# Optimization experiments

Measured on AMD Instinct MI355X. Metric: run time of the kernel, lower is better.

The kernel has to match this reference:

```python
import jax, jax.numpy as jnp
import numpy as np

NG, N, NFG, NFR, NFP, B = 4, 64, 1024, 256, 256, 2048
SCALE = 1.0 / float(np.sqrt(NFR + NFP))
EPS = 1e-5  # torch LayerNorm default


def setup_inputs() -> dict:
    key = jax.random.key(0)
    k = jax.random.split(key, 4)
    x = jax.random.normal(k[0], (B, N, NFG), dtype=jnp.float32)
    # per-graph params stacked over NG for vectorized computation
    Wt = jax.random.normal(k[1], (NG, NFR, NFG), dtype=jnp.float32) * 0.02
    bt = jnp.zeros((NG, NFR), dtype=jnp.float32)
    Wp = jax.random.normal(k[2], (NG, NFR, NFG), dtype=jnp.float32) * 0.02
    bp = jnp.zeros((NG, NFR), dtype=jnp.float32)
    Wg = jax.random.normal(k[3], (NG, NFG, NFG), dtype=jnp.float32) * 0.02  # [out,in]
    gamma = jnp.ones((NG, NFG), dtype=jnp.float32)
    beta = jnp.zeros((NG, NFG), dtype=jnp.float32)
    return {"x": x, "Wt": Wt, "bt": bt, "Wp": Wp, "bp": bp,
            "Wg": Wg, "gamma": gamma, "beta": beta}


def reference(x, Wt, bt, Wp, bp, Wg, gamma, beta):
    # theta/phi projections, vectorized over NG graphs: [G,B,N,R]
    theta = jnp.einsum('bnf,grf->gbnr', x, Wt) + bt[:, None, None, :]
    phi = jnp.einsum('bnf,grf->gbnr', x, Wp) + bp[:, None, None, :]
    # original computes sim=theta@phi^T then .sum(2); identical math:
    # relation[b,n] = theta[b,n] . sum_m phi[b,m]  (avoids the NxN matrix)
    phi_sum = phi.sum(axis=2)                                  # [G,B,R]
    relation = jnp.einsum('gbnr,gbr->gbn', theta, phi_sum) * SCALE
    w = jax.nn.softmax(relation, axis=2)                       # softmax over boxes N
    # attention-weighted aggregation over boxes -> [G,B,NFG]
    agg = jnp.einsum('gbn,bnf->gbf', w, x)
    # GCN linear (no bias): [G,B,NFG]
    h = jnp.einsum('gbf,gof->gbo', agg, Wg)
    # LayerNorm over feature dim, per graph
    mu = h.mean(axis=-1, keepdims=True)
    var = ((h - mu) ** 2).mean(axis=-1, keepdims=True)
    h = (h - mu) * jax.lax.rsqrt(var + EPS) * gamma[:, None, :] + beta[:, None, :]
    h = jax.nn.relu(h)
    # mean over the NG graphs; restore keepdim axis -> [B,1,NFG]
    return h.mean(axis=0)[:, None, :]
```

## Files before the change

kernel.cpp:

```cpp
#include <hip/hip_runtime.h>
#include <hip/hip_bf16.h>

typedef __attribute__((ext_vector_type(4))) float f4;
typedef __attribute__((ext_vector_type(4))) float f32x4;
typedef __attribute__((ext_vector_type(8))) short short8;
typedef __attribute__((ext_vector_type(2))) unsigned int u32x2;
typedef __attribute__((ext_vector_type(4))) unsigned int u32x4;
typedef unsigned int u32;
typedef unsigned short u16;

#define SCALE_F 0.04419417382415922f

__device__ inline u16 f2bf(float f) {
  u32 u = __float_as_uint(f);
  u32 r = u + 0x7FFFu + ((u >> 16) & 1u);
  return (u16)(r >> 16);
}
__device__ inline float bflo(u32 u) { return __uint_as_float(u << 16); }
__device__ inline float bfhi(u32 u) { return __uint_as_float(u & 0xFFFF0000u); }

#define GLD16(gsrc, ldst)                                                     \
  __builtin_amdgcn_global_load_lds(                                           \
      (const __attribute__((address_space(1))) void*)(gsrc),                  \
      (__attribute__((address_space(3))) void*)(ldst), 16, 0, 0)

__global__ __launch_bounds__(256) void k0_cvt(const float* __restrict__ src,
                                              u16* __restrict__ dst) {
  int i = blockIdx.x * 256 + threadIdx.x;
  const f4* s = (const f4*)src;
  f4 a = s[(size_t)i * 2];
  f4 b = s[(size_t)i * 2 + 1];
  u32x4 p;
  p[0] = (u32)f2bf(a[0]) | ((u32)f2bf(a[1]) << 16);
  p[1] = (u32)f2bf(a[2]) | ((u32)f2bf(a[3]) << 16);
  p[2] = (u32)f2bf(b[0]) | ((u32)f2bf(b[1]) << 16);
  p[3] = (u32)f2bf(b[2]) | ((u32)f2bf(b[3]) << 16);
  *(u32x4*)(dst + (size_t)i * 8) = p;
}

__global__ __launch_bounds__(256) void k0_wt(const float* __restrict__ Wt,
                                             u16* __restrict__ Wtt) {
  const int g = blockIdx.z;
  const int f0 = blockIdx.x * 64, r0 = blockIdx.y * 64;
  __shared__ u16 tile[64][66];
  const int t = threadIdx.x;
  const float* src = Wt + ((size_t)g * 256 + r0) * 1024 + f0;
#pragma unroll
  for (int i = 0; i < 16; ++i) {
    int idx = t + i * 256;
    int rl = idx >> 6, fl = idx & 63;
    tile[fl][rl] = f2bf(src[rl * 1024 + fl]);
  }
  __syncthreads();
  u16* dst = Wtt + ((size_t)g * 1024 + f0) * 256 + r0;
#pragma unroll
  for (int i = 0; i < 4; ++i) {
    int idx = t + i * 256;
    int fl = idx >> 4, rq = idx & 15;
    u32x2 p;
    p[0] = (u32)tile[fl][rq * 4]     | ((u32)tile[fl][rq * 4 + 1] << 16);
    p[1] = (u32)tile[fl][rq * 4 + 2] | ((u32)tile[fl][rq * 4 + 3] << 16);
    *(u32x2*)(dst + fl * 256 + rq * 4) = p;
  }
}

__global__ __launch_bounds__(256) void k1_prep(const float* __restrict__ x,
                                               u16* __restrict__ xs16,
                                               char* __restrict__ xpre) {
  const int b = blockIdx.x, t = threadIdx.x;
  const float* xb = x + (size_t)b * 65536;
  char* xp = xpre + (size_t)b * 131072;
  const int slot = t >> 1, half = t & 1;
  f4 acc = {0.f, 0.f, 0.f, 0.f};
#pragma unroll 8
  for (int n = 0; n < 64; ++n) {
    f4 v = *(const f4*)(xb + n * 1024 + t * 4);
    acc += v;
    u32 p0 = (u32)f2bf(v[0]) | ((u32)f2bf(v[1]) << 16);
    u32 p1 = (u32)f2bf(v[2]) | ((u32)f2bf(v[3]) << 16);
    char* dst = xp + n * 2048 + ((slot ^ (n & 7)) << 4) + half * 8;
    ((u32*)dst)[0] = p0;
    ((u32*)dst)[1] = p1;
  }
  u32x2 p;
  p[0] = (u32)f2bf(acc[0]) | ((u32)f2bf(acc[1]) << 16);
  p[1] = (u32)f2bf(acc[2]) | ((u32)f2bf(acc[3]) << 16);
  *(u32x2*)(xs16 + (size_t)b * 1024 + t * 4) = p;
}

__global__ __launch_bounds__(256) void k2_gemm(const u16* __restrict__ A,
                                               const u16* __restrict__ Bt,
                                               const float* __restrict__ bp,
                                               u16* __restrict__ C) {
  const int n0 = blockIdx.x * 128, m0 = blockIdx.y * 128;
  __shared__ u16 Al[128 * 32];
  __shared__ u16 Bl[128 * 32];
  const int t = threadIdx.x;
  const int w = t >> 6, l = t & 63;
  const int wr = w >> 1, wc = w & 1;
  const int lr = l & 15, lh = l >> 4;
  f32x4 acc[4][4] = {};
  for (int kt = 0; kt < 1024; kt += 32) {
#pragma unroll
    for (int j = 0; j < 2; ++j) {
      int idx = t + j * 256;
      int row = idx >> 2, sl = idx & 3;
      GLD16(A + (size_t)(m0 + row) * 1024 + kt + sl * 8, Al + idx * 8);
      GLD16(Bt + (size_t)(n0 + row) * 1024 + kt + sl * 8, Bl + idx * 8);
    }
    __syncthreads();
    short8 af[4], bfr[4];
#pragma unroll
    for (int m = 0; m < 4; ++m)
      af[m] = *(const short8*)(Al + (wr * 64 + m * 16 + lr) * 32 + lh * 8);
#pragma unroll
    for (int n = 0; n < 4; ++n)
      bfr[n] = *(const short8*)(Bl + (wc * 64 + n * 16 + lr) * 32 + lh * 8);
#pragma unroll
    for (int m = 0; m < 4; ++m)
#pragma unroll
      for (int n = 0; n < 4; ++n)
        acc[m][n] = __builtin_amdgcn_mfma_f32_16x16x32_bf16(af[m], bfr[n],
                                                            acc[m][n], 0, 0, 0);
    __syncthreads();
  }
#pragma unroll
  for (int m = 0; m < 4; ++m)
#pragma unroll
    for (int n = 0; n < 4; ++n) {
      int col = n0 + wc * 64 + n * 16 + lr;
      float bb = 64.0f * bp[col];
#pragma unroll
      for (int j = 0; j < 4; ++j)
        C[(size_t)(m0 + wr * 64 + m * 16 + lh * 4 + j) * 1024 + col] =
            f2bf(acc[m][n][j] + bb);
    }
}

__global__ __launch_bounds__(256) void k3_gemm(const u16* __restrict__ A,
                                               const u16* __restrict__ Btt,
                                               u16* __restrict__ Vb) {
  const int g = blockIdx.z;
  const int n0 = blockIdx.x * 128, m0 = blockIdx.y * 128;
  const u16* Bg = Btt + (size_t)g * 1024 * 256;
  __shared__ u16 Al[128 * 32];
  __shared__ u16 Bl[128 * 32];
  const int t = threadIdx.x;
  const int w = t >> 6, l = t & 63;
  const int wr = w >> 1, wc = w & 1;
  const int lr = l & 15, lh = l >> 4;
  f32x4 acc[4][4] = {};
  for (int kt = 0; kt < 256; kt += 32) {
#pragma unroll
    for (int j = 0; j < 2; ++j) {
      int idx = t + j * 256;
      int row = idx >> 2, sl = idx & 3;
      GLD16(A + (size_t)(m0 + row) * 1024 + g * 256 + kt + sl * 8, Al + idx * 8);
      GLD16(Bg + (size_t)(n0 + row) * 256 + kt + sl * 8, Bl + idx * 8);
    }
    __syncthreads();
    short8 af[4], bfr[4];
#pragma unroll
    for (int m = 0; m < 4; ++m)
      af[m] = *(const short8*)(Al + (wr * 64 + m * 16 + lr) * 32 + lh * 8);
#pragma unroll
    for (int n = 0; n < 4; ++n)
      bfr[n] = *(const short8*)(Bl + (wc * 64 + n * 16 + lr) * 32 + lh * 8);
#pragma unroll
    for (int m = 0; m < 4; ++m)
#pragma unroll
      for (int n = 0; n < 4; ++n)
        acc[m][n] = __builtin_amdgcn_mfma_f32_16x16x32_bf16(af[m], bfr[n],
                                                            acc[m][n], 0, 0, 0);
    __syncthreads();
  }
  u16* Vg = Vb + (size_t)g * 2048 * 1024;
#pragma unroll
  for (int m = 0; m < 4; ++m)
#pragma unroll
    for (int n = 0; n < 4; ++n)
#pragma unroll
      for (int j = 0; j < 4; ++j)
        Vg[(size_t)(m0 + wr * 64 + m * 16 + lh * 4 + j) * 1024 +
           (n0 + wc * 64 + n * 16 + lr)] = f2bf(acc[m][n][j]);
}

__device__ __forceinline__ void relation_phase(const char* xl, const u16* vb,
                                               float* relp, int w, int l) {
  const int lg = l >> 4, lr = l & 15;
  f32x4 racc[4] = {};
#pragma unroll
  for (int kp = 0; kp < 2; ++kp) {
    const int kt = kp * 512 + w * 32;
    short8 afr = {};
    if (lr < 4) afr = *(const short8*)(vb + lr * 1032 + kt + lg * 8);
#pragma unroll
    for (int nt = 0; nt < 4; ++nt) {
      int n = nt * 16 + lr;
      short8 bfrg = *(const short8*)(
          xl + n * 2048 + ((((kt >> 3) + lg) ^ (n & 7)) << 4));
      racc[nt] = __builtin_amdgcn_mfma_f32_16x16x32_bf16(afr, bfrg, racc[nt],
                                                         0, 0, 0);
    }
  }
  if (l < 16) {
#pragma unroll
    for (int nt = 0; nt < 4; ++nt)
#pragma unroll
      for (int j = 0; j < 4; ++j)
        relp[(w * 4 + j) * 64 + nt * 16 + lr] = racc[nt][j];
  }
}

__device__ __forceinline__ void softmax_phase(const float* relp, float* wsm,
                                              int t) {
  if (t < 256) {
    const int g = t >> 6, n = t & 63;
    float rel = 0.f;
#pragma unroll
    for (int ww = 0; ww < 16; ++ww) rel += relp[(ww * 4 + g) * 64 + n];
    rel *= SCALE_F;
    float mx = rel;
#pragma unroll
    for (int o = 32; o > 0; o >>= 1) mx = fmaxf(mx, __shfl_xor(mx, o, 64));
    float e = __expf(rel - mx);
    float s = e;
#pragma unroll
    for (int o = 32; o > 0; o >>= 1) s += __shfl_xor(s, o, 64);
    wsm[t] = e / s;
  }
}

__device__ __forceinline__ void agg_phase(const char* xl, const float* wsm,
                                          float* relp, u16* aggb, int b,
                                          int t) {
  const int hh = t >> 9, r = t & 511, g = r >> 7, f8 = r & 127;
  const float* wg = wsm + g * 64 + hh * 32;
  float a0 = 0, a1 = 0, a2 = 0, a3 = 0, a4 = 0, a5 = 0, a6 = 0, a7 = 0;
#pragma unroll 8
  for (int n0 = 0; n0 < 32; ++n0) {
    int n = hh * 32 + n0;
    float wv = wg[n0];
    u32x4 xp = *(const u32x4*)(xl + n * 2048 + ((f8 ^ (n & 7)) << 4));
    a0 = fmaf(bflo(xp[0]), wv, a0);
    a1 = fmaf(bfhi(xp[0]), wv, a1);
    a2 = fmaf(bflo(xp[1]), wv, a2);
    a3 = fmaf(bfhi(xp[1]), wv, a3);
    a4 = fmaf(bflo(xp[2]), wv, a4);
    a5 = fmaf(bfhi(xp[2]), wv, a5);
    a6 = fmaf(bflo(xp[3]), wv, a6);
    a7 = fmaf(bfhi(xp[3]), wv, a7);
  }
  if (hh) {
    f4 q0 = {a0, a1, a2, a3};
    f4 q1 = {a4, a5, a6, a7};
    *(f4*)(relp + r * 8) = q0;
    *(f4*)(relp + r * 8 + 4) = q1;
  }
  __syncthreads();
  if (!hh) {
    f4 q0 = *(const f4*)(relp + r * 8);
    f4 q1 = *(const f4*)(relp + r * 8 + 4);
    u32x4 p;
    p[0] = (u32)f2bf(a0 + q0[0]) | ((u32)f2bf(a1 + q0[1]) << 16);
    p[1] = (u32)f2bf(a2 + q0[2]) | ((u32)f2bf(a3 + q0[3]) << 16);
    p[2] = (u32)f2bf(a4 + q1[0]) | ((u32)f2bf(a5 + q1[1]) << 16);
    p[3] = (u32)f2bf(a6 + q1[2]) | ((u32)f2bf(a7 + q1[3]) << 16);
    *(u32x4*)(aggb + ((size_t)g * 2048 + b) * 1024 + f8 * 8) = p;
  }
}

#define K4_LDS (131072 + 8256 + 16384 + 1024)
__global__ __launch_bounds__(1024) void k4_fused(const char* __restrict__ xpre,
                                                 const u16* __restrict__ vb16,
                                                 u16* __restrict__ aggb) {
  extern __shared__ char sm[];
  char* xl = sm;
  u16* vb = (u16*)(sm + 131072);
  float* relp = (float*)(sm + 131072 + 8256);
  float* wsm = (float*)(sm + 131072 + 8256 + 16384);
  const int t = threadIdx.x;
  const int w = t >> 6, l = t & 63;
  const int b0 = blockIdx.x * 2, b1 = b0 + 1;

  {
    int g = t >> 8, q = t & 255;
    u32x2 pv = *(const u32x2*)(vb16 + ((size_t)g * 2048 + b0) * 1024 + q * 4);
    *(u32x2*)(vb + g * 1032 + q * 4) = pv;
  }
  const char* xg0 = xpre + (size_t)b0 * 131072;
#pragma unroll
  for (int i = 0; i < 8; ++i)
    GLD16(xg0 + (w * 8 + i) * 1024 + l * 16, xl + (w * 8 + i) * 1024 + l * 16);
  __syncthreads();

  const char* xg1 = xpre + (size_t)b1 * 131072;
  u32x4 pf0 = *(const u32x4*)(xg1 + t * 16);
  u32x4 pf1 = *(const u32x4*)(xg1 + t * 16 + 16384);
  u32x4 pf2 = *(const u32x4*)(xg1 + t * 16 + 32768);
  u32x4 pf3 = *(const u32x4*)(xg1 + t * 16 + 49152);
  u32x4 pf4 = *(const u32x4*)(xg1 + t * 16 + 65536);
  u32x4 pf5 = *(const u32x4*)(xg1 + t * 16 + 81920);
  u32x4 pf6 = *(const u32x4*)(xg1 + t * 16 + 98304);
  u32x4 pf7 = *(const u32x4*)(xg1 + t * 16 + 114688);
  u32x2 pv1 =
      *(const u32x2*)(vb16 + ((size_t)(t >> 8) * 2048 + b1) * 1024 + (t & 255) * 4);

  relation_phase(xl, vb, relp, w, l);
  __syncthreads();
  softmax_phase(relp, wsm, t);
  __syncthreads();
  agg_phase(xl, wsm, relp, aggb, b0, t);
  __syncthreads();

  *(u32x4*)(xl + t * 16) = pf0;
  *(u32x4*)(xl + t * 16 + 16384) = pf1;
  *(u32x4*)(xl + t * 16 + 32768) = pf2;
  *(u32x4*)(xl + t * 16 + 49152) = pf3;
  *(u32x4*)(xl + t * 16 + 65536) = pf4;
  *(u32x4*)(xl + t * 16 + 81920) = pf5;
  *(u32x4*)(xl + t * 16 + 98304) = pf6;
  *(u32x4*)(xl + t * 16 + 114688) = pf7;
  {
    int g = t >> 8, q = t & 255;
    *(u32x2*)(vb + g * 1032 + q * 4) = pv1;
  }
  __syncthreads();

  relation_phase(xl, vb, relp, w, l);
  __syncthreads();
  softmax_phase(relp, wsm, t);
  __syncthreads();
  agg_phase(xl, wsm, relp, aggb, b1, t);
}

__global__ __launch_bounds__(256) void k5_gemm(const u16* __restrict__ Ab,
                                               const u16* __restrict__ Bb,
                                               u16* __restrict__ H) {
  const int g = blockIdx.z;
  const int n0 = blockIdx.x * 128, m0 = blockIdx.y * 128;
  const u16* A = Ab + (size_t)g * 2048 * 1024;
  const u16* Bt = Bb + (size_t)g * 1024 * 1024;
  __shared__ u16 Al[128 * 32];
  __shared__ u16 Bl[128 * 32];
  const int t = threadIdx.x;
  const int w = t >> 6, l = t & 63;
  const int wr = w >> 1, wc = w & 1;
  const int lr = l & 15, lh = l >> 4;
  f32x4 acc[4][4] = {};
  for (int kt = 0; kt < 1024; kt += 32) {
#pragma unroll
    for (int j = 0; j < 2; ++j) {
      int idx = t + j * 256;
      int row = idx >> 2, sl = idx & 3;
      GLD16(A + (size_t)(m0 + row) * 1024 + kt + sl * 8, Al + idx * 8);
      GLD16(Bt + (size_t)(n0 + row) * 1024 + kt + sl * 8, Bl + idx * 8);
    }
    __syncthreads();
    short8 af[4], bfr[4];
#pragma unroll
    for (int m = 0; m < 4; ++m)
      af[m] = *(const short8*)(Al + (wr * 64 + m * 16 + lr) * 32 + lh * 8);
#pragma unroll
    for (int n = 0; n < 4; ++n)
      bfr[n] = *(const short8*)(Bl + (wc * 64 + n * 16 + lr) * 32 + lh * 8);
#pragma unroll
    for (int m = 0; m < 4; ++m)
#pragma unroll
      for (int n = 0; n < 4; ++n)
        acc[m][n] = __builtin_amdgcn_mfma_f32_16x16x32_bf16(af[m], bfr[n],
                                                            acc[m][n], 0, 0, 0);
    __syncthreads();
  }
  u16* Hg = H + (size_t)g * 2048 * 1024;
#pragma unroll
  for (int m = 0; m < 4; ++m)
#pragma unroll
    for (int n = 0; n < 4; ++n)
#pragma unroll
      for (int j = 0; j < 4; ++j)
        Hg[(size_t)(m0 + wr * 64 + m * 16 + lh * 4 + j) * 1024 +
           (n0 + wc * 64 + n * 16 + lr)] = f2bf(acc[m][n][j]);
}

__global__ __launch_bounds__(256) void k6_ln(const u16* __restrict__ H,
                                             const float* __restrict__ gamma,
                                             const float* __restrict__ beta,
                                             float* __restrict__ out) {
  const int b = blockIdx.x, t = threadIdx.x;
  const int w = t >> 6, lane = t & 63;
  __shared__ float red[8];
  f4 acc = {0.f, 0.f, 0.f, 0.f};
  for (int g = 0; g < 4; ++g) {
    u32x2 hp = *(const u32x2*)(H + ((size_t)g * 2048 + b) * 1024 + t * 4);
    f4 hv = {bflo(hp[0]), bfhi(hp[0]), bflo(hp[1]), bfhi(hp[1])};
    float s = hv[0] + hv[1] + hv[2] + hv[3];
    float q = hv[0] * hv[0] + hv[1] * hv[1] + hv[2] * hv[2] + hv[3] * hv[3];
#pragma unroll
    for (int o = 32; o > 0; o >>= 1) {
      s += __shfl_xor(s, o, 64);
      q += __shfl_xor(q, o, 64);
    }
    if (lane == 0) { red[w] = s; red[4 + w] = q; }
    __syncthreads();
    s = red[0] + red[1] + red[2] + red[3];
    q = red[4] + red[5] + red[6] + red[7];
    float mean = s * (1.f / 1024.f);
    float var = q * (1.f / 1024.f) - mean * mean;
    float rstd = rsqrtf(var + 1e-5f);
    f4 gm = *(const f4*)(gamma + g * 1024 + t * 4);
    f4 bt = *(const f4*)(beta + g * 1024 + t * 4);
#pragma unroll
    for (int j = 0; j < 4; ++j) {
      float val = (hv[j] - mean) * rstd * gm[j] + bt[j];
      acc[j] += fmaxf(val, 0.f);
    }
    __syncthreads();
  }
  acc *= 0.25f;
  *(f4*)(out + (size_t)b * 1024 + t * 4) = acc;
}

extern "C" void kernel_launch(void* const* d_in, const int* in_sizes, int n_in,
                              void* d_out, int out_size, void* d_ws, size_t ws_size,
                              hipStream_t stream) {
  const float* x     = (const float*)d_in[0];
  const float* Wt    = (const float*)d_in[1];
  const float* Wp    = (const float*)d_in[3];
  const float* bp    = (const float*)d_in[4];
  const float* Wg    = (const float*)d_in[5];
  const float* gamma = (const float*)d_in[6];
  const float* beta  = (const float*)d_in[7];
  float* out = (float*)d_out;

  char* ws = (char*)d_ws;
  u16*   xs16 = (u16*)(ws);
  u16*   ps16 = (u16*)(ws + (4u << 20));
  u16*   wpb  = (u16*)(ws + (8u << 20));
  u16*   wtb  = (u16*)(ws + (10u << 20));
  u16*   wgb  = (u16*)(ws + (12u << 20));
  u16*   vb16 = (u16*)(ws + (20u << 20));
  u16*   aggb = (u16*)(ws + (36u << 20));
  u16*   hb16 = (u16*)(ws + (52u << 20));
  char*  xpre = (char*)(ws + (68u << 20));

  hipFuncSetAttribute((const void*)k4_fused,
                      hipFuncAttributeMaxDynamicSharedMemorySize, K4_LDS);

  k0_cvt<<<2048, 256, 0, stream>>>(Wg, wgb);
  k0_cvt<<<512, 256, 0, stream>>>(Wp, wpb);
  k0_wt<<<dim3(16, 4, 4), 256, 0, stream>>>(Wt, wtb);
  k1_prep<<<2048, 256, 0, stream>>>(x, xs16, xpre);
  k2_gemm<<<dim3(8, 16), 256, 0, stream>>>(xs16, wpb, bp, ps16);
  k3_gemm<<<dim3(8, 16, 4), 256, 0, stream>>>(ps16, wtb, vb16);
  k4_fused<<<1024, 1024, K4_LDS, stream>>>(xpre, vb16, aggb);
  k5_gemm<<<dim3(8, 16, 4), 256, 0, stream>>>(aggb, wgb, hb16);
  k6_ln<<<2048, 256, 0, stream>>>(hb16, gamma, beta, out);
}
```

Baseline: 346.6 us.

## Merge weight-conversion kernels, shrink k2 tile for more blocks, reverse k4 order

The three weight-conversion launches become a single kernel that dispatches on block index, saving launch overhead. The k2 GEMM tile narrows from 128x128 to 128x64, doubling its grid from 128 to 256 blocks so more CUs are busy on this 2048x1024 problem. The k4 block-to-batch mapping is reversed, likely so the most recently written xpre data is read first while it may still be in cache. The narrower tile reloads the A operand more often.

```diff
diff --git a/kernel.cpp b/kernel.cpp
--- a/kernel.cpp
+++ b/kernel.cpp
@@ -24,9 +24,9 @@
       (const __attribute__((address_space(1))) void*)(gsrc),                  \
       (__attribute__((address_space(3))) void*)(ldst), 16, 0, 0)
 
-__global__ __launch_bounds__(256) void k0_cvt(const float* __restrict__ src,
-                                              u16* __restrict__ dst) {
-  int i = blockIdx.x * 256 + threadIdx.x;
+__device__ __forceinline__ void cvt8(const float* __restrict__ src,
+                                     u16* __restrict__ dst, int blk, int t) {
+  int i = blk * 256 + t;
   const f4* s = (const f4*)src;
   f4 a = s[(size_t)i * 2];
   f4 b = s[(size_t)i * 2 + 1];
@@ -38,29 +38,40 @@
   *(u32x4*)(dst + (size_t)i * 8) = p;
 }
 
-__global__ __launch_bounds__(256) void k0_wt(const float* __restrict__ Wt,
-                                             u16* __restrict__ Wtt) {
-  const int g = blockIdx.z;
-  const int f0 = blockIdx.x * 64, r0 = blockIdx.y * 64;
-  __shared__ u16 tile[64][66];
-  const int t = threadIdx.x;
-  const float* src = Wt + ((size_t)g * 256 + r0) * 1024 + f0;
-#pragma unroll
-  for (int i = 0; i < 16; ++i) {
-    int idx = t + i * 256;
-    int rl = idx >> 6, fl = idx & 63;
-    tile[fl][rl] = f2bf(src[rl * 1024 + fl]);
-  }
-  __syncthreads();
-  u16* dst = Wtt + ((size_t)g * 1024 + f0) * 256 + r0;
-#pragma unroll
-  for (int i = 0; i < 4; ++i) {
-    int idx = t + i * 256;
-    int fl = idx >> 4, rq = idx & 15;
-    u32x2 p;
-    p[0] = (u32)tile[fl][rq * 4]     | ((u32)tile[fl][rq * 4 + 1] << 16);
-    p[1] = (u32)tile[fl][rq * 4 + 2] | ((u32)tile[fl][rq * 4 + 3] << 16);
-    *(u32x2*)(dst + fl * 256 + rq * 4) = p;
+__global__ __launch_bounds__(256) void k0_prep(const float* __restrict__ Wg,
+                                               const float* __restrict__ Wp,
+                                               const float* __restrict__ Wt,
+                                               u16* __restrict__ wgb,
+                                               u16* __restrict__ wpb,
+                                               u16* __restrict__ wtb) {
+  const int blk = blockIdx.x, t = threadIdx.x;
+  if (blk < 2048) {
+    cvt8(Wg, wgb, blk, t);
+  } else if (blk < 2560) {
+    cvt8(Wp, wpb, blk - 2048, t);
+  } else {
+    __shared__ u16 tile[64][66];
+    const int bid = blk - 2560;
+    const int g = bid >> 6, rem = bid & 63;
+    const int f0 = (rem & 15) * 64, r0 = (rem >> 4) * 64;
+    const float* src = Wt + ((size_t)g * 256 + r0) * 1024 + f0;
+#pragma unroll
+    for (int i = 0; i < 16; ++i) {
+      int idx = t + i * 256;
+      int rl = idx >> 6, fl = idx & 63;
+      tile[fl][rl] = f2bf(src[rl * 1024 + fl]);
+    }
+    __syncthreads();
+    u16* dst = wtb + ((size_t)g * 1024 + f0) * 256 + r0;
+#pragma unroll
+    for (int i = 0; i < 4; ++i) {
+      int idx = t + i * 256;
+      int fl = idx >> 4, rq = idx & 15;
+      u32x2 p;
+      p[0] = (u32)tile[fl][rq * 4]     | ((u32)tile[fl][rq * 4 + 1] << 16);
+      p[1] = (u32)tile[fl][rq * 4 + 2] | ((u32)tile[fl][rq * 4 + 3] << 16);
+      *(u32x2*)(dst + fl * 256 + rq * 4) = p;
+    }
   }
 }
 
@@ -92,32 +103,34 @@
                                                const u16* __restrict__ Bt,
                                                const float* __restrict__ bp,
                                                u16* __restrict__ C) {
-  const int n0 = blockIdx.x * 128, m0 = blockIdx.y * 128;
+  const int n0 = blockIdx.x * 64, m0 = blockIdx.y * 128;
   __shared__ u16 Al[128 * 32];
-  __shared__ u16 Bl[128 * 32];
+  __shared__ u16 Bl[64 * 32];
   const int t = threadIdx.x;
   const int w = t >> 6, l = t & 63;
-  const int wr = w >> 1, wc = w & 1;
   const int lr = l & 15, lh = l >> 4;
-  f32x4 acc[4][4] = {};
+  f32x4 acc[2][4] = {};
   for (int kt = 0; kt < 1024; kt += 32) {
 #pragma unroll
     for (int j = 0; j < 2; ++j) {
       int idx = t + j * 256;
       int row = idx >> 2, sl = idx & 3;
       GLD16(A + (size_t)(m0 + row) * 1024 + kt + sl * 8, Al + idx * 8);
-      GLD16(Bt + (size_t)(n0 + row) * 1024 + kt + sl * 8, Bl + idx * 8);
-    }
-    __syncthreads();
-    short8 af[4], bfr[4];
-#pragma unroll
-    for (int m = 0; m < 4; ++m)
-      af[m] = *(const short8*)(Al + (wr * 64 + m * 16 + lr) * 32 + lh * 8);
+    }
+    {
+      int row = t >> 2, sl = t & 3;
+      GLD16(Bt + (size_t)(n0 + row) * 1024 + kt + sl * 8, Bl + t * 8);
+    }
+    __syncthreads();
+    short8 af[2], bfr[4];
+#pragma unroll
+    for (int m = 0; m < 2; ++m)
+      af[m] = *(const short8*)(Al + (w * 32 + m * 16 + lr) * 32 + lh * 8);
 #pragma unroll
     for (int n = 0; n < 4; ++n)
-      bfr[n] = *(const short8*)(Bl + (wc * 64 + n * 16 + lr) * 32 + lh * 8);
-#pragma unroll
-    for (int m = 0; m < 4; ++m)
+      bfr[n] = *(const short8*)(Bl + (n * 16 + lr) * 32 + lh * 8);
+#pragma unroll
+    for (int m = 0; m < 2; ++m)
 #pragma unroll
       for (int n = 0; n < 4; ++n)
         acc[m][n] = __builtin_amdgcn_mfma_f32_16x16x32_bf16(af[m], bfr[n],
@@ -125,14 +138,14 @@
     __syncthreads();
   }
 #pragma unroll
-  for (int m = 0; m < 4; ++m)
+  for (int m = 0; m < 2; ++m)
 #pragma unroll
     for (int n = 0; n < 4; ++n) {
-      int col = n0 + wc * 64 + n * 16 + lr;
+      int col = n0 + n * 16 + lr;
       float bb = 64.0f * bp[col];
 #pragma unroll
       for (int j = 0; j < 4; ++j)
-        C[(size_t)(m0 + wr * 64 + m * 16 + lh * 4 + j) * 1024 + col] =
+        C[(size_t)(m0 + w * 32 + m * 16 + lh * 4 + j) * 1024 + col] =
             f2bf(acc[m][n][j] + bb);
     }
 }
@@ -281,7 +294,7 @@
   float* wsm = (float*)(sm + 131072 + 8256 + 16384);
   const int t = threadIdx.x;
   const int w = t >> 6, l = t & 63;
-  const int b0 = blockIdx.x * 2, b1 = b0 + 1;
+  const int b0 = (1023 - blockIdx.x) * 2, b1 = b0 + 1;
 
   {
     int g = t >> 8, q = t & 255;
@@ -447,11 +460,9 @@
   hipFuncSetAttribute((const void*)k4_fused,
                       hipFuncAttributeMaxDynamicSharedMemorySize, K4_LDS);
 
-  k0_cvt<<<2048, 256, 0, stream>>>(Wg, wgb);
-  k0_cvt<<<512, 256, 0, stream>>>(Wp, wpb);
-  k0_wt<<<dim3(16, 4, 4), 256, 0, stream>>>(Wt, wtb);
+  k0_prep<<<2816, 256, 0, stream>>>(Wg, Wp, Wt, wgb, wpb, wtb);
   k1_prep<<<2048, 256, 0, stream>>>(x, xs16, xpre);
-  k2_gemm<<<dim3(8, 16), 256, 0, stream>>>(xs16, wpb, bp, ps16);
+  k2_gemm<<<dim3(16, 16), 256, 0, stream>>>(xs16, wpb, bp, ps16);
   k3_gemm<<<dim3(8, 16, 4), 256, 0, stream>>>(ps16, wtb, vb16);
   k4_fused<<<1024, 1024, K4_LDS, stream>>>(xpre, vb16, aggb);
   k5_gemm<<<dim3(8, 16, 4), 256, 0, stream>>>(aggb, wgb, hb16);
```

After: 336.1 us. 1.03x faster.
